# Kernel optimization log

Measured on AMD Instinct MI355X. Metric: run time of the kernel, lower is better.

## Reference

```python
import jax, jax.numpy as jnp
import numpy as np

EPS = 1e-8

def spatial_similarity(x):
    # x: [B, C, H, W] -> similarity [B, 1, HW, HW]
    b, c = x.shape[0], x.shape[1]
    fm = x.reshape(b, c, -1)                                   # [B, C, HW]
    norm_fm = fm / (jnp.sqrt(jnp.sum(fm * fm, axis=1, keepdims=True)) + EPS)
    s = jnp.einsum('bcn,bcm->bnm', norm_fm, norm_fm)            # [B, HW, HW]
    return s[:, None]                                           # [B, 1, HW, HW]

def l1_loss(a, b):
    return jnp.mean(jnp.abs(a - b))

def setup_inputs() -> dict:
    key = jax.random.key(0)
    k0, k1, k2, k3 = jax.random.split(key, 4)
    shape = (8, 128, 48, 48)
    return {
        'outputs0': jax.random.normal(k0, shape, dtype=jnp.float32),
        'outputs1': jax.random.normal(k1, shape, dtype=jnp.float32),
        'targets0': jax.random.normal(k2, shape, dtype=jnp.float32),
        'targets1': jax.random.normal(k3, shape, dtype=jnp.float32),
    }

def reference(outputs0, outputs1, targets0, targets1):
    # stu_ch == tea_ch -> random index slice is identity (index = 0)
    loss = l1_loss(spatial_similarity(outputs0), spatial_similarity(targets0))
    loss = loss + l1_loss(spatial_similarity(outputs1), spatial_similarity(targets1))
    return loss
```

## Files before the change

### kernel.cpp

```cpp
#include <hip/hip_runtime.h>
#include <hip/hip_bf16.h>
#include <stdint.h>

#define B_DIM 8
#define C_DIM 128
#define N_SP 2304
#define NT 18
#define NTRI 171

typedef __attribute__((ext_vector_type(8))) short short8;
typedef __attribute__((ext_vector_type(4))) float f32x4;

__device__ __forceinline__ uint32_t f2bf(float f) {
    uint32_t u = __float_as_uint(f);
    return (u + 0x7fffu + ((u >> 16) & 1u)) >> 16;
}

__global__ __launch_bounds__(256) void prep_kernel(
    const float* __restrict__ x0, const float* __restrict__ x1,
    const float* __restrict__ x2, const float* __restrict__ x3,
    ushort* __restrict__ xt, float* __restrict__ rinv)
{
    int bid = blockIdx.x;
    int t  = bid / 72;
    int b  = (bid / 9) % 8;
    int n  = (bid % 9) * 256 + threadIdx.x;
    const float* x  = t == 0 ? x0 : t == 1 ? x1 : t == 2 ? x2 : x3;
    const float* xb = x + (size_t)b * (C_DIM * N_SP) + n;
    ushort* row = xt + ((size_t)(t * 8 + b) * N_SP + n) * 128;
    int sw = n & 7;
    float s = 0.f;
#pragma unroll
    for (int c = 0; c < 4; ++c) {
        uint32_t w[16];
#pragma unroll
        for (int m = 0; m < 16; ++m) {
            float v0 = xb[(size_t)(c * 32 + 2 * m) * N_SP];
            float v1 = xb[(size_t)(c * 32 + 2 * m + 1) * N_SP];
            s = fmaf(v0, v0, s);
            s = fmaf(v1, v1, s);
            w[m] = f2bf(v0) | (f2bf(v1) << 16);
        }
#pragma unroll
        for (int j = 0; j < 4; ++j) {
            uint4 u; u.x = w[4*j]; u.y = w[4*j+1]; u.z = w[4*j+2]; u.w = w[4*j+3];
            *(uint4*)(row + (((c * 4 + j) ^ sw) * 8)) = u;
        }
    }
    rinv[(size_t)(t * 8 + b) * N_SP + n] = 1.f / (sqrtf(s) + 1e-8f);
}

#define STAGE(xsrc, h)                                                              \
    {                                                                               \
        const ushort* sb = (wid & 2) ? (xsrc) + (size_t)tm * 16384                  \
                                     : (xsrc) + (size_t)tn * 16384;                 \
        ushort* pp = (wid & 2) ? pB : pA;                                           \
        int i0 = (wid & 1) * 8;                                                     \
        _Pragma("unroll")                                                           \
        for (int i = 0; i < 8; ++i) {                                               \
            int ii = i0 + i;                                                        \
            int col = ii * 8 + (lane >> 3);                                         \
            const ushort* src = sb + (size_t)col * 128 + (h) * 64 + (lane & 7) * 8; \
            __builtin_amdgcn_global_load_lds(                                       \
                (const __attribute__((address_space(1))) uint32_t*)src,             \
                (__attribute__((address_space(3))) uint32_t*)(pp + ii * 512),       \
                16, 0, 0);                                                          \
        }                                                                           \
    }

#define COMPUTE(ACC)                                                                \
    _Pragma("unroll")                                                               \
    for (int s = 0; s < 2; ++s) {                                                   \
        short8 av[4], bv[4];                                                        \
        int g = lane >> 4;                                                          \
        _Pragma("unroll")                                                           \
        for (int i = 0; i < 4; ++i) {                                               \
            int ca = wrow * 64 + i * 16 + (lane & 15);                              \
            av[i] = *(const short8*)&pA[ca * 64 + ((s * 4 + g) ^ (ca & 7)) * 8];    \
            int cb = wcol * 64 + i * 16 + (lane & 15);                              \
            bv[i] = *(const short8*)&pB[cb * 64 + ((s * 4 + g) ^ (cb & 7)) * 8];    \
        }                                                                           \
        _Pragma("unroll")                                                           \
        for (int i = 0; i < 4; ++i)                                                 \
            _Pragma("unroll")                                                       \
            for (int j = 0; j < 4; ++j)                                             \
                ACC[i][j] = __builtin_amdgcn_mfma_f32_16x16x32_bf16(                \
                    av[i], bv[j], ACC[i][j], 0, 0, 0);                              \
    }

__global__ __launch_bounds__(256, 2) void gram_kernel(
    const ushort* __restrict__ xt, const float* __restrict__ rinv,
    float* __restrict__ accum)
{
    __shared__ ushort pA[128 * 64];
    __shared__ ushort pB[128 * 64];
    __shared__ float rn[4][128];
    __shared__ float wred[4];

    int bid  = blockIdx.x;
    int pair = bid / (B_DIM * NTRI);
    int rem  = bid - pair * (B_DIM * NTRI);
    int b    = rem / NTRI;
    int t    = rem - b * NTRI;
    int tn = 0, cnt = NT;
    while (t >= cnt) { t -= cnt; --cnt; ++tn; }
    int tm = tn + t;

    const ushort* xo = xt + (size_t)(pair * 8 + b) * N_SP * 128;
    const ushort* xg = xt + (size_t)((pair + 2) * 8 + b) * N_SP * 128;
    const float*  ro = rinv + (size_t)(pair * 8 + b) * N_SP;
    const float*  rg = rinv + (size_t)((pair + 2) * 8 + b) * N_SP;

    int tid  = threadIdx.x;
    int wid  = tid >> 6;
    int lane = tid & 63;
    int wrow = wid >> 1, wcol = wid & 1;

    f32x4 acc_o[4][4], acc_t[4][4];
#pragma unroll
    for (int i = 0; i < 4; ++i)
#pragma unroll
        for (int j = 0; j < 4; ++j) {
            acc_o[i][j] = (f32x4){0.f, 0.f, 0.f, 0.f};
            acc_t[i][j] = (f32x4){0.f, 0.f, 0.f, 0.f};
        }

    STAGE(xo, 0);
    if (tid < 128) {
        rn[0][tid] = ro[tn * 128 + tid];
        rn[1][tid] = ro[tm * 128 + tid];
    } else {
        int q = tid - 128;
        rn[2][q] = rg[tn * 128 + q];
        rn[3][q] = rg[tm * 128 + q];
    }
    __syncthreads();
    COMPUTE(acc_o);
    __syncthreads();
    STAGE(xo, 1);
    __syncthreads();
    COMPUTE(acc_o);
    __syncthreads();
    STAGE(xg, 0);
    __syncthreads();
    COMPUTE(acc_t);
    __syncthreads();
    STAGE(xg, 1);
    __syncthreads();
    COMPUTE(acc_t);

    int fr = lane & 15, fq = lane >> 4;
    float co[4], cg[4];
#pragma unroll
    for (int j = 0; j < 4; ++j) {
        co[j] = rn[1][wcol * 64 + j * 16 + fr];
        cg[j] = rn[3][wcol * 64 + j * 16 + fr];
    }
    float w2 = (tn == tm) ? 1.f : 2.f;
    float lsum = 0.f;
#pragma unroll
    for (int i = 0; i < 4; ++i) {
#pragma unroll
        for (int r = 0; r < 4; ++r) {
            int rowl = wrow * 64 + i * 16 + fq * 4 + r;
            float ror = rn[0][rowl], rgr = rn[2][rowl];
#pragma unroll
            for (int j = 0; j < 4; ++j) {
                float so = acc_o[i][j][r] * ror * co[j];
                float st = acc_t[i][j][r] * rgr * cg[j];
                lsum += fabsf(so - st);
            }
        }
    }
    lsum *= w2;
#pragma unroll
    for (int off = 32; off > 0; off >>= 1) lsum += __shfl_down(lsum, off, 64);
    if (lane == 0) wred[wid] = lsum;
    __syncthreads();
    if (tid == 0) atomicAdd(&accum[pair], wred[0] + wred[1] + wred[2] + wred[3]);
}

__global__ void finalize_kernel(const float* __restrict__ a, float* __restrict__ out) {
    out[0] = (a[0] + a[1]) * (1.0f / 42467328.0f);
}

extern "C" void kernel_launch(void* const* d_in, const int* in_sizes, int n_in,
                              void* d_out, int out_size, void* d_ws, size_t ws_size,
                              hipStream_t stream) {
    const float* o0 = (const float*)d_in[0];
    const float* o1 = (const float*)d_in[1];
    const float* t0 = (const float*)d_in[2];
    const float* t1 = (const float*)d_in[3];

    ushort* xtw  = (ushort*)d_ws;
    float*  rinv = (float*)((char*)d_ws + (size_t)4 * 8 * N_SP * 256);
    float*  accum = rinv + 4 * 8 * N_SP;

    hipMemsetAsync(accum, 0, 2 * sizeof(float), stream);
    prep_kernel<<<288, 256, 0, stream>>>(o0, o1, t0, t1, xtw, rinv);
    gram_kernel<<<2 * B_DIM * NTRI, 256, 0, stream>>>(xtw, rinv, accum);
    finalize_kernel<<<1, 1, 0, stream>>>(accum, (float*)d_out);
}
```

Before: 143.8 us.

## Double-buffer gram staging, restructure prep with LDS, spread atomics and remap blocks

The gram kernel now uses two LDS buffers so the next global-to-LDS load is issued before computing on the current one, cutting the number of barriers. The prep kernel splits each column's channels across 4 threads, stages the bf16 rows in LDS and writes them out coalesced, giving 4x more blocks. Block indices are permuted across the 8 XCDs, and the final atomics are spread over 32 slots per pair, with finalize summing 64 values. The trade-off is double the LDS in gram_kernel, which may limit occupancy.

```diff
diff --git a/kernel.cpp b/kernel.cpp
--- a/kernel.cpp
+++ b/kernel.cpp
@@ -7,6 +7,7 @@
 #define N_SP 2304
 #define NT 18
 #define NTRI 171
+#define GRID_G (2 * B_DIM * NTRI)
 
 typedef __attribute__((ext_vector_type(8))) short short8;
 typedef __attribute__((ext_vector_type(4))) float f32x4;
@@ -21,40 +22,53 @@
     const float* __restrict__ x2, const float* __restrict__ x3,
     ushort* __restrict__ xt, float* __restrict__ rinv)
 {
+    __shared__ ushort stage[64 * 128];
+
     int bid = blockIdx.x;
-    int t  = bid / 72;
-    int b  = (bid / 9) % 8;
-    int n  = (bid % 9) * 256 + threadIdx.x;
+    int t  = bid / 288;
+    int b  = (bid / 36) % 8;
+    int nb = bid % 36;
+    int tid = threadIdx.x;
+    int q   = tid & 3;
+    int nl  = tid >> 2;
+    int n   = nb * 64 + nl;
     const float* x  = t == 0 ? x0 : t == 1 ? x1 : t == 2 ? x2 : x3;
     const float* xb = x + (size_t)b * (C_DIM * N_SP) + n;
-    ushort* row = xt + ((size_t)(t * 8 + b) * N_SP + n) * 128;
-    int sw = n & 7;
+    int sw = nl & 7;
+
     float s = 0.f;
 #pragma unroll
-    for (int c = 0; c < 4; ++c) {
-        uint32_t w[16];
-#pragma unroll
-        for (int m = 0; m < 16; ++m) {
-            float v0 = xb[(size_t)(c * 32 + 2 * m) * N_SP];
-            float v1 = xb[(size_t)(c * 32 + 2 * m + 1) * N_SP];
+    for (int jj = 0; jj < 4; ++jj) {
+        uint32_t w[4];
+#pragma unroll
+        for (int m = 0; m < 4; ++m) {
+            int c = q * 32 + jj * 8 + m * 2;
+            float v0 = xb[(size_t)c * N_SP];
+            float v1 = xb[(size_t)(c + 1) * N_SP];
             s = fmaf(v0, v0, s);
             s = fmaf(v1, v1, s);
             w[m] = f2bf(v0) | (f2bf(v1) << 16);
         }
-#pragma unroll
-        for (int j = 0; j < 4; ++j) {
-            uint4 u; u.x = w[4*j]; u.y = w[4*j+1]; u.z = w[4*j+2]; u.w = w[4*j+3];
-            *(uint4*)(row + (((c * 4 + j) ^ sw) * 8)) = u;
-        }
-    }
-    rinv[(size_t)(t * 8 + b) * N_SP + n] = 1.f / (sqrtf(s) + 1e-8f);
-}
-
-#define STAGE(xsrc, h)                                                              \
+        int J = q * 4 + jj;
+        uint4 u; u.x = w[0]; u.y = w[1]; u.z = w[2]; u.w = w[3];
+        *(uint4*)&stage[nl * 128 + ((J ^ sw) * 8)] = u;
+    }
+    s += __shfl_xor(s, 1, 64);
+    s += __shfl_xor(s, 2, 64);
+    if (q == 0) rinv[(size_t)(t * 8 + b) * N_SP + n] = 1.f / (sqrtf(s) + 1e-8f);
+
+    __syncthreads();
+    ushort* dst = xt + ((size_t)(t * 8 + b) * N_SP + (size_t)nb * 64) * 128;
+#pragma unroll
+    for (int it = 0; it < 4; ++it)
+        *(uint4*)(dst + it * 2048 + tid * 8) = *(const uint4*)(stage + it * 2048 + tid * 8);
+}
+
+#define STAGE(xsrc, h, PA, PB)                                                      \
     {                                                                               \
         const ushort* sb = (wid & 2) ? (xsrc) + (size_t)tm * 16384                  \
                                      : (xsrc) + (size_t)tn * 16384;                 \
-        ushort* pp = (wid & 2) ? pB : pA;                                           \
+        ushort* pp = (wid & 2) ? (PB) : (PA);                                       \
         int i0 = (wid & 1) * 8;                                                     \
         _Pragma("unroll")                                                           \
         for (int i = 0; i < 8; ++i) {                                               \
@@ -68,7 +82,7 @@
         }                                                                           \
     }
 
-#define COMPUTE(ACC)                                                                \
+#define COMPUTE(ACC, PA, PB)                                                        \
     _Pragma("unroll")                                                               \
     for (int s = 0; s < 2; ++s) {                                                   \
         short8 av[4], bv[4];                                                        \
@@ -76,9 +90,9 @@
         _Pragma("unroll")                                                           \
         for (int i = 0; i < 4; ++i) {                                               \
             int ca = wrow * 64 + i * 16 + (lane & 15);                              \
-            av[i] = *(const short8*)&pA[ca * 64 + ((s * 4 + g) ^ (ca & 7)) * 8];    \
+            av[i] = *(const short8*)&(PA)[ca * 64 + ((s * 4 + g) ^ (ca & 7)) * 8];  \
             int cb = wcol * 64 + i * 16 + (lane & 15);                              \
-            bv[i] = *(const short8*)&pB[cb * 64 + ((s * 4 + g) ^ (cb & 7)) * 8];    \
+            bv[i] = *(const short8*)&(PB)[cb * 64 + ((s * 4 + g) ^ (cb & 7)) * 8];  \
         }                                                                           \
         _Pragma("unroll")                                                           \
         for (int i = 0; i < 4; ++i)                                                 \
@@ -92,12 +106,14 @@
     const ushort* __restrict__ xt, const float* __restrict__ rinv,
     float* __restrict__ accum)
 {
-    __shared__ ushort pA[128 * 64];
-    __shared__ ushort pB[128 * 64];
+    __shared__ ushort pA[2][128 * 64];
+    __shared__ ushort pB[2][128 * 64];
     __shared__ float rn[4][128];
     __shared__ float wred[4];
 
-    int bid  = blockIdx.x;
+    int bid0 = blockIdx.x;
+    int bid  = (bid0 & 7) * (GRID_G / 8) + (bid0 >> 3);
+
     int pair = bid / (B_DIM * NTRI);
     int rem  = bid - pair * (B_DIM * NTRI);
     int b    = rem / NTRI;
@@ -125,7 +141,7 @@
             acc_t[i][j] = (f32x4){0.f, 0.f, 0.f, 0.f};
         }
 
-    STAGE(xo, 0);
+    STAGE(xo, 0, pA[0], pB[0]);
     if (tid < 128) {
         rn[0][tid] = ro[tn * 128 + tid];
         rn[1][tid] = ro[tm * 128 + tid];
@@ -135,19 +151,16 @@
         rn[3][q] = rg[tm * 128 + q];
     }
     __syncthreads();
-    COMPUTE(acc_o);
-    __syncthreads();
-    STAGE(xo, 1);
-    __syncthreads();
-    COMPUTE(acc_o);
-    __syncthreads();
-    STAGE(xg, 0);
-    __syncthreads();
-    COMPUTE(acc_t);
-    __syncthreads();
-    STAGE(xg, 1);
-    __syncthreads();
-    COMPUTE(acc_t);
+    STAGE(xo, 1, pA[1], pB[1]);
+    COMPUTE(acc_o, pA[0], pB[0]);
+    __syncthreads();
+    STAGE(xg, 0, pA[0], pB[0]);
+    COMPUTE(acc_o, pA[1], pB[1]);
+    __syncthreads();
+    STAGE(xg, 1, pA[1], pB[1]);
+    COMPUTE(acc_t, pA[0], pB[0]);
+    __syncthreads();
+    COMPUTE(acc_t, pA[1], pB[1]);
 
     int fr = lane & 15, fq = lane >> 4;
     float co[4], cg[4];
@@ -177,11 +190,14 @@
     for (int off = 32; off > 0; off >>= 1) lsum += __shfl_down(lsum, off, 64);
     if (lane == 0) wred[wid] = lsum;
     __syncthreads();
-    if (tid == 0) atomicAdd(&accum[pair], wred[0] + wred[1] + wred[2] + wred[3]);
+    if (tid == 0)
+        atomicAdd(&accum[pair * 32 + (bid0 & 31)], wred[0] + wred[1] + wred[2] + wred[3]);
 }
 
 __global__ void finalize_kernel(const float* __restrict__ a, float* __restrict__ out) {
-    out[0] = (a[0] + a[1]) * (1.0f / 42467328.0f);
+    float s = 0.f;
+    for (int i = 0; i < 64; ++i) s += a[i];
+    out[0] = s * (1.0f / 42467328.0f);
 }
 
 extern "C" void kernel_launch(void* const* d_in, const int* in_sizes, int n_in,
@@ -196,8 +212,8 @@
     float*  rinv = (float*)((char*)d_ws + (size_t)4 * 8 * N_SP * 256);
     float*  accum = rinv + 4 * 8 * N_SP;
 
-    hipMemsetAsync(accum, 0, 2 * sizeof(float), stream);
-    prep_kernel<<<288, 256, 0, stream>>>(o0, o1, t0, t1, xtw, rinv);
-    gram_kernel<<<2 * B_DIM * NTRI, 256, 0, stream>>>(xtw, rinv, accum);
+    hipMemsetAsync(accum, 0, 64 * sizeof(float), stream);
+    prep_kernel<<<1152, 256, 0, stream>>>(o0, o1, t0, t1, xtw, rinv);
+    gram_kernel<<<GRID_G, 256, 0, stream>>>(xtw, rinv, accum);
     finalize_kernel<<<1, 1, 0, stream>>>(accum, (float*)d_out);
 }
```

Measured after the change: 126.3 us. -12.2%, faster.
